# Performance work log

Measured on AMD Instinct MI355X. Metric: run time of the kernel, lower is better.

## Reference

```python
import jax, jax.numpy as jnp
import numpy as np

B, S, V, E, H, L = 2, 2048, 32000, 512, 8, 4
DH = E // H      # 64 head dim
M = 256          # FAVOR+ random features
CHUNK = 128      # causal prefix-sum chunk size


def setup_inputs() -> dict:
    key = jax.random.key(0)
    ks = jax.random.split(key, 12)
    init = lambda k, shape, s=0.02: (jax.random.normal(k, shape) * s).astype(jnp.float32)
    return {
        "src": jax.random.randint(ks[0], (B, S), 0, V),
        "tgt": jax.random.randint(ks[1], (B, S), 0, V),
        "emb": init(ks[2], (V, E), 1.0),
        "ln_emb_g": jnp.ones((E,), jnp.float32), "ln_emb_b": jnp.zeros((E,), jnp.float32),
        "Wq": init(ks[3], (L, E, E)), "Wk": init(ks[4], (L, E, E)),
        "Wv": init(ks[5], (L, E, E)), "Wo": init(ks[6], (L, E, E)),
        "ln1_g": jnp.ones((L, E), jnp.float32), "ln1_b": jnp.zeros((L, E), jnp.float32),
        "W1": init(ks[7], (L, E, 4 * E)), "b1": jnp.zeros((L, 4 * E), jnp.float32),
        "W2": init(ks[8], (L, 4 * E, E)), "b2": jnp.zeros((L, E), jnp.float32),
        "ln2_g": jnp.ones((L, E), jnp.float32), "ln2_b": jnp.zeros((L, E), jnp.float32),
        "proj": jax.random.normal(ks[9], (L, M, DH), dtype=jnp.float32),  # FAVOR+ projections (buffers)
        "fc_w": init(ks[10], (E, V)), "fc_b": jnp.zeros((V,), jnp.float32),
    }


def _ln(x, g, b, eps=1e-5):
    mu = jnp.mean(x, -1, keepdims=True)
    var = jnp.mean((x - mu) ** 2, -1, keepdims=True)
    return (x - mu) * jax.lax.rsqrt(var + eps) * g + b


def _posenc(s, e):
    pos = jnp.arange(s, dtype=jnp.float32)[:, None]
    div = jnp.exp(jnp.arange(0, e, 2, dtype=jnp.float32) * (-jnp.log(10000.0) / e))
    ang = pos * div                                   # [s, e/2]
    return jnp.stack([jnp.sin(ang), jnp.cos(ang)], -1).reshape(s, e)


def _features(x, proj, is_query):
    # FAVOR+ positive softmax-kernel random features. x: [b,h,s,d], proj: [m,d]
    dn = x.shape[-1] ** -0.25
    ratio = proj.shape[0] ** -0.5
    xd = jnp.einsum('bhsd,md->bhsm', x, proj) * dn
    diag = 0.5 * jnp.sum((x * dn) ** 2, -1)[..., None]
    mx = jnp.max(xd, -1, keepdims=True) if is_query else jnp.max(xd)
    return ratio * (jnp.exp(xd - diag - mx) + 1e-4)


def _causal_linear_attn(q, k, v):
    # q,k: [b,h,s,m] positive features; v: [b,h,s,d]. Chunked prefix-sum recurrence.
    b, h, s, m = q.shape
    d = v.shape[-1]
    nc = s // CHUNK
    rs = lambda t: t.reshape(b, h, nc, CHUNK, t.shape[-1]).transpose(2, 0, 1, 3, 4)

    def step(carry, inp):
        Ssum, zsum = carry                             # [b,h,m,d], [b,h,m]
        qc, kc, vc = inp                               # [b,h,c,m/ d]
        kv = jnp.einsum('bhcm,bhcd->bhcmd', kc, vc)
        Sc = Ssum[:, :, None] + jnp.cumsum(kv, axis=2)
        zc = zsum[:, :, None] + jnp.cumsum(kc, axis=2)
        num = jnp.einsum('bhcm,bhcmd->bhcd', qc, Sc)
        den = jnp.einsum('bhcm,bhcm->bhc', qc, zc)
        return (Sc[:, :, -1], zc[:, :, -1]), num / (den[..., None] + 1e-6)

    init = (jnp.zeros((b, h, m, d), q.dtype), jnp.zeros((b, h, m), q.dtype))
    _, outs = jax.lax.scan(step, init, (rs(q), rs(k), rs(v)))
    return outs.transpose(1, 2, 0, 3, 4).reshape(b, h, s, d)


def _forward(src, tgt, emb, ln_emb_g, ln_emb_b, Wq, Wk, Wv, Wo, ln1_g, ln1_b,
             W1, b1, W2, b2, ln2_g, ln2_b, proj, fc_w, fc_b):
    s = src.shape[1]
    pe = _posenc(s, E)
    x = emb[src] + pe                                 # [B,S,E]
    # tgt is embedded+normed in the original wrapper but the encoder-style Performer
    # only consumes its first (src) argument; masks default to None.
    _ = _ln(emb[tgt] + pe[: tgt.shape[1]], ln_emb_g, ln_emb_b)
    x = _ln(x, ln_emb_g, ln_emb_b)

    def layer(x, p):
        wq, wk, wv, wo, g1, bb1, w1, c1, w2, c2, g2, bb2, P = p
        h = _ln(x, g1, bb1)
        bsz, sl = h.shape[0], h.shape[1]
        split = lambda t: t.reshape(bsz, sl, H, DH).transpose(0, 2, 1, 3)  # [b,h,s,dh]
        q, k, v = split(h @ wq), split(h @ wk), split(h @ wv)
        qf = _features(q, P, True)
        kf = _features(k, P, False)
        o = _causal_linear_attn(qf, kf, v)
        o = o.transpose(0, 2, 1, 3).reshape(bsz, sl, E)
        x = x + o @ wo
        h2 = _ln(x, g2, bb2)
        x = x + jax.nn.gelu(h2 @ w1 + c1, approximate=False) @ w2 + c2
        return x, None

    x, _ = jax.lax.scan(layer, x, (Wq, Wk, Wv, Wo, ln1_g, ln1_b, W1, b1, W2, b2, ln2_g, ln2_b, proj))
    return x @ fc_w + fc_b                             # [B,S,V]


def reference(src, tgt, emb, ln_emb_g, ln_emb_b, Wq, Wk, Wv, Wo, ln1_g, ln1_b,
              W1, b1, W2, b2, ln2_g, ln2_b, proj, fc_w, fc_b):
    return _forward(src, tgt, emb, ln_emb_g, ln_emb_b, Wq, Wk, Wv, Wo, ln1_g, ln1_b,
                    W1, b1, W2, b2, ln2_g, ln2_b, proj, fc_w, fc_b)
```

## Files before the change

kernel.cpp:

```cpp
#include <hip/hip_runtime.h>
#include <math.h>

typedef unsigned short u16;
typedef unsigned int u32;
typedef __attribute__((ext_vector_type(8))) short bf16x8;
typedef __attribute__((ext_vector_type(4))) float f32x4;

constexpr int B_  = 2;
constexpr int S_  = 2048;
constexpr int V_  = 32000;
constexpr int E_  = 512;
constexpr int H_  = 8;
constexpr int L_  = 4;
constexpr int DH_ = 64;
constexpr int M_  = 256;
constexpr int CH_ = 128;
constexpr int NC_ = 16;
constexpr int NTOK_ = B_ * S_;
constexpr int KE_ = 3 * E_;
constexpr int KF_ = 3 * 4 * E_;

__device__ __forceinline__ float warp_sum64(float x) {
#pragma unroll
  for (int off = 32; off; off >>= 1) x += __shfl_xor(x, off);
  return x;
}
__device__ __forceinline__ float warp_max64(float x) {
#pragma unroll
  for (int off = 32; off; off >>= 1) x = fmaxf(x, __shfl_xor(x, off));
  return x;
}
__device__ __forceinline__ u16 bf16_rne(float x) {
  u32 u = __builtin_bit_cast(u32, x);
  u += 0x7fffu + ((u >> 16) & 1u);
  return (u16)(u >> 16);
}
__device__ __forceinline__ float bf16_f(u16 h) {
  u32 u = ((u32)h) << 16;
  return __builtin_bit_cast(float, u);
}
__device__ __forceinline__ void gload_lds16(const u16* g, u16* l) {
  __builtin_amdgcn_global_load_lds(
      (const __attribute__((address_space(1))) void*)g,
      (__attribute__((address_space(3))) void*)l, 16, 0, 0);
}
__device__ __forceinline__ void ext_write(u16* ro, int col, int seg, float v) {
  const u16 hi = bf16_rne(v);
  const u16 lo = bf16_rne(v - bf16_f(hi));
  ro[col] = hi; ro[seg + col] = hi; ro[2 * seg + col] = lo;
}

__global__ __launch_bounds__(256) void embed_ln_k(
    const int* __restrict__ src, const float* __restrict__ emb,
    const float* __restrict__ g, const float* __restrict__ bta,
    float* __restrict__ X) {
  __shared__ float red[4];
  const int row = blockIdx.x;
  const int s   = row & (S_ - 1);
  const int tid = threadIdx.x;
  const int tok = src[row];
  float v[2];
#pragma unroll
  for (int i = 0; i < 2; i++) {
    const int e = tid + i * 256;
    const float j = (float)(e & ~1);
    const float div = expf(j * (-9.210340371976184f / (float)E_));
    const float ang = (float)s * div;
    const float pe = (e & 1) ? cosf(ang) : sinf(ang);
    v[i] = emb[(size_t)tok * E_ + e] + pe;
  }
  float sum = warp_sum64(v[0] + v[1]);
  if ((tid & 63) == 0) red[tid >> 6] = sum;
  __syncthreads();
  const float mu = (red[0] + red[1] + red[2] + red[3]) * (1.f / E_);
  __syncthreads();
  const float d0 = v[0] - mu, d1 = v[1] - mu;
  float s2 = warp_sum64(d0 * d0 + d1 * d1);
  if ((tid & 63) == 0) red[tid >> 6] = s2;
  __syncthreads();
  const float var = (red[0] + red[1] + red[2] + red[3]) * (1.f / E_);
  const float r = rsqrtf(var + 1e-5f);
  X[(size_t)row * E_ + tid]       = d0 * r * g[tid] + bta[tid];
  X[(size_t)row * E_ + tid + 256] = d1 * r * g[tid + 256] + bta[tid + 256];
}

__global__ __launch_bounds__(256) void ln_rows_ext_k(
    const float* __restrict__ Xin, const float* __restrict__ g,
    const float* __restrict__ bta, u16* __restrict__ Eo) {
  __shared__ float red[4];
  const int row = blockIdx.x, tid = threadIdx.x;
  const float* xr = Xin + (size_t)row * E_;
  const float v0 = xr[tid], v1 = xr[tid + 256];
  float sum = warp_sum64(v0 + v1);
  if ((tid & 63) == 0) red[tid >> 6] = sum;
  __syncthreads();
  const float mu = (red[0] + red[1] + red[2] + red[3]) * (1.f / E_);
  __syncthreads();
  const float d0 = v0 - mu, d1 = v1 - mu;
  float s2 = warp_sum64(d0 * d0 + d1 * d1);
  if ((tid & 63) == 0) red[tid >> 6] = s2;
  __syncthreads();
  const float var = (red[0] + red[1] + red[2] + red[3]) * (1.f / E_);
  const float r = rsqrtf(var + 1e-5f);
  u16* ro = Eo + (size_t)row * KE_;
  ext_write(ro, tid,       E_, d0 * r * g[tid] + bta[tid]);
  ext_write(ro, tid + 256, E_, d1 * r * g[tid + 256] + bta[tid + 256]);
}

__global__ __launch_bounds__(256) void xconv_k(
    const float* __restrict__ X, u16* __restrict__ Eo) {
  const int row = blockIdx.x, tid = threadIdx.x;
  u16* ro = Eo + (size_t)row * KE_;
#pragma unroll
  for (int i = 0; i < 2; i++) {
    const int e = tid + i * 256;
    ext_write(ro, e, E_, X[(size_t)row * E_ + e]);
  }
}

__global__ __launch_bounds__(256) void convw_k(
    const float* __restrict__ W, u16* __restrict__ D, int K, int ldsrc) {
  __shared__ float t[32][33];
  const int tid = threadIdx.x;
  const int n0 = blockIdx.x * 32, k0 = blockIdx.y * 32;
  const int r = tid >> 5, c = tid & 31;
#pragma unroll
  for (int i = 0; i < 4; i++)
    t[r + i * 8][c] = W[(size_t)(k0 + r + i * 8) * ldsrc + n0 + c];
  __syncthreads();
#pragma unroll
  for (int i = 0; i < 4; i++) {
    const int nn = r + i * 8;
    const float v = t[c][nn];
    const u16 hi = bf16_rne(v);
    const u16 lo = bf16_rne(v - bf16_f(hi));
    u16* ro = D + (size_t)(n0 + nn) * (3 * K) + k0 + c;
    ro[0] = hi; ro[K] = lo; ro[2 * K] = hi;
  }
}

__global__ __launch_bounds__(256) void convw4_k(
    const float* __restrict__ p0, const float* __restrict__ p1,
    const float* __restrict__ p2, const float* __restrict__ p3,
    u16* __restrict__ D) {
  __shared__ float t[32][33];
  const int tid = threadIdx.x, z = blockIdx.z;
  const float* ps[4] = {p0, p1, p2, p3};
  const float* W = ps[z];
  u16* Dz = D + (size_t)z * E_ * KE_;
  const int n0 = blockIdx.x * 32, k0 = blockIdx.y * 32;
  const int r = tid >> 5, c = tid & 31;
#pragma unroll
  for (int i = 0; i < 4; i++)
    t[r + i * 8][c] = W[(size_t)(k0 + r + i * 8) * E_ + n0 + c];
  __syncthreads();
#pragma unroll
  for (int i = 0; i < 4; i++) {
    const int nn = r + i * 8;
    const float v = t[c][nn];
    const u16 hi = bf16_rne(v);
    const u16 lo = bf16_rne(v - bf16_f(hi));
    u16* ro = Dz + (size_t)(n0 + nn) * KE_ + k0 + c;
    ro[0] = hi; ro[E_] = lo; ro[2 * E_] = hi;
  }
}

template <int BM, bool BIAS, bool ACC, bool GEXT>
__global__ __launch_bounds__(256) void gemm_bf3(
    const u16* __restrict__ A, const u16* __restrict__ Bt,
    const float* __restrict__ bias, float* __restrict__ C,
    u16* __restrict__ Eo, int Kp, int ldC, int NE) {
  constexpr int BN = 128, BK = 64;
  constexpr int WROWS = BM / 64;
  constexpr int WCOLS = 4 / WROWS;
  constexpr int CW = BN / WCOLS;
  constexpr int MR = 4;
  constexpr int NR = CW / 16;
  __shared__ u16 Al[BM * BK];
  __shared__ u16 Bl[BN * BK];
  const int tid = threadIdx.x;
  const int wid = tid >> 6, lane = tid & 63;
  const int wr = wid / WCOLS, wc = wid % WCOLS;
  const int l15 = lane & 15, l4 = lane >> 4;
  const int bm = blockIdx.y * BM, bn = blockIdx.x * BN;
  f32x4 acc[MR][NR];
#pragma unroll
  for (int i = 0; i < MR; i++)
#pragma unroll
    for (int j = 0; j < NR; j++) acc[i][j] = (f32x4)(0.f);
  const int srow = tid >> 3;
  const int scol = (tid & 7) * 8;
  const u16* Abase = A + (size_t)(bm + srow) * Kp + scol;
  const u16* Bbase = Bt + (size_t)(bn + srow) * Kp + scol;
  for (int k0 = 0; k0 < Kp; k0 += BK) {
#pragma unroll
    for (int i = 0; i < BM / 32; i++)
      gload_lds16(Abase + (size_t)(i * 32) * Kp + k0, Al + i * 2048 + tid * 8);
#pragma unroll
    for (int i = 0; i < 4; i++)
      gload_lds16(Bbase + (size_t)(i * 32) * Kp + k0, Bl + i * 2048 + tid * 8);
    __syncthreads();
#pragma unroll
    for (int kk = 0; kk < BK; kk += 32) {
      bf16x8 af[MR], bfr[NR];
#pragma unroll
      for (int i = 0; i < MR; i++)
        af[i] = *reinterpret_cast<const bf16x8*>(
            &Al[(wr * 64 + i * 16 + l15) * BK + kk + l4 * 8]);
#pragma unroll
      for (int j = 0; j < NR; j++)
        bfr[j] = *reinterpret_cast<const bf16x8*>(
            &Bl[(wc * CW + j * 16 + l15) * BK + kk + l4 * 8]);
#pragma unroll
      for (int i = 0; i < MR; i++)
#pragma unroll
        for (int j = 0; j < NR; j++)
          acc[i][j] = __builtin_amdgcn_mfma_f32_16x16x32_bf16(
              af[i], bfr[j], acc[i][j], 0, 0, 0);
    }
    __syncthreads();
  }
#pragma unroll
  for (int i = 0; i < MR; i++) {
#pragma unroll
    for (int j = 0; j < NR; j++) {
#pragma unroll
      for (int r = 0; r < 4; r++) {
        const int row = bm + wr * 64 + i * 16 + l4 * 4 + r;
        const int col = bn + wc * CW + j * 16 + l15;
        float v = acc[i][j][r];
        if constexpr (BIAS) v += bias[col];
        if constexpr (GEXT) {
          v = 0.5f * v * (1.f + erff(v * 0.7071067811865475f));
          ext_write(Eo + (size_t)row * (3 * NE), col, NE, v);
        } else {
          const size_t ci = (size_t)row * ldC + col;
          if constexpr (ACC) C[ci] += v; else C[ci] = v;
        }
      }
    }
  }
}

__global__ __launch_bounds__(256) void feat_q_k(
    const float* __restrict__ Q, const float* __restrict__ P,
    float* __restrict__ QF) {
  __shared__ alignas(16) float qrow[64];
  __shared__ float red[4];
  const int tid = threadIdx.x, bx = blockIdx.x;
  const int st = bx & 255, h = (bx >> 8) & 7, b = bx >> 11;
  float4 preg[16];
#pragma unroll
  for (int i = 0; i < 16; i++)
    preg[i] = *reinterpret_cast<const float4*>(&P[(size_t)tid * DH_ + i * 4]);
  const float dn = 0.35355339059327373f;
  for (int ss = 0; ss < 8; ss++) {
    const int s = st * 8 + ss;
    if (tid < 64) qrow[tid] = Q[((size_t)(b * S_ + s)) * E_ + h * DH_ + tid];
    __syncthreads();
    float xd = 0.f, q2 = 0.f;
#pragma unroll
    for (int i = 0; i < 16; i++) {
      const float4 q4 = *reinterpret_cast<const float4*>(&qrow[i * 4]);
      xd += preg[i].x * q4.x + preg[i].y * q4.y + preg[i].z * q4.z + preg[i].w * q4.w;
      q2 += q4.x * q4.x + q4.y * q4.y + q4.z * q4.z + q4.w * q4.w;
    }
    xd *= dn;
    const float dg = 0.5f * dn * dn * q2;
    float mx = warp_max64(xd);
    if ((tid & 63) == 0) red[tid >> 6] = mx;
    __syncthreads();
    mx = fmaxf(fmaxf(red[0], red[1]), fmaxf(red[2], red[3]));
    QF[(((size_t)(b * H_ + h)) * S_ + s) * M_ + tid] =
        0.0625f * (expf(xd - dg - mx) + 1e-4f);
    __syncthreads();
  }
}

__global__ __launch_bounds__(256) void feat_k1_k(
    const float* __restrict__ K, const float* __restrict__ P,
    float* __restrict__ KF, float* __restrict__ DIAGK, float* __restrict__ PMAX) {
  __shared__ alignas(16) float krow[64];
  __shared__ float red[4];
  const int tid = threadIdx.x, bx = blockIdx.x;
  const int st = bx & 255, h = (bx >> 8) & 7, b = bx >> 11;
  float4 preg[16];
#pragma unroll
  for (int i = 0; i < 16; i++)
    preg[i] = *reinterpret_cast<const float4*>(&P[(size_t)tid * DH_ + i * 4]);
  const float dn = 0.35355339059327373f;
  float bmax = -3.0e38f;
  for (int ss = 0; ss < 8; ss++) {
    const int s = st * 8 + ss;
    if (tid < 64) krow[tid] = K[((size_t)(b * S_ + s)) * E_ + h * DH_ + tid];
    __syncthreads();
    float xd = 0.f, q2 = 0.f;
#pragma unroll
    for (int i = 0; i < 16; i++) {
      const float4 q4 = *reinterpret_cast<const float4*>(&krow[i * 4]);
      xd += preg[i].x * q4.x + preg[i].y * q4.y + preg[i].z * q4.z + preg[i].w * q4.w;
      q2 += q4.x * q4.x + q4.y * q4.y + q4.z * q4.z + q4.w * q4.w;
    }
    xd *= dn;
    const float dg = 0.5f * dn * dn * q2;
    const size_t ridx = ((size_t)(b * H_ + h)) * S_ + s;
    KF[ridx * M_ + tid] = xd;
    if (tid == 0) DIAGK[ridx] = dg;
    bmax = fmaxf(bmax, xd);
    __syncthreads();
  }
  bmax = warp_max64(bmax);
  if ((tid & 63) == 0) red[tid >> 6] = bmax;
  __syncthreads();
  if (tid == 0) PMAX[bx] = fmaxf(fmaxf(red[0], red[1]), fmaxf(red[2], red[3]));
}

__global__ __launch_bounds__(256) void maxred_k(
    const float* __restrict__ PM, int n, float* __restrict__ G) {
  __shared__ float w[4];
  const int tid = threadIdx.x;
  float v = -3.0e38f;
  for (int i = tid; i < n; i += 256) v = fmaxf(v, PM[i]);
  v = warp_max64(v);
  if ((tid & 63) == 0) w[tid >> 6] = v;
  __syncthreads();
  if (tid == 0) G[0] = fmaxf(fmaxf(w[0], w[1]), fmaxf(w[2], w[3]));
}

__global__ __launch_bounds__(256) void feat_k2_k(
    float* __restrict__ KF, const float* __restrict__ DIAG,
    const float* __restrict__ G) {
  const float gm = G[0];
  const size_t n = (size_t)B_ * H_ * S_ * M_;
  for (size_t i = (size_t)blockIdx.x * 256 + threadIdx.x; i < n;
       i += (size_t)gridDim.x * 256) {
    const float xd = KF[i];
    const float dg = DIAG[i >> 8];
    KF[i] = 0.0625f * (expf(xd - dg - gm) + 1e-4f);
  }
}

__global__ __launch_bounds__(256) void chunk_sums_k(
    const float* __restrict__ KF, const float* __restrict__ V,
    float* __restrict__ CSKV, float* __restrict__ CSZ) {
  __shared__ alignas(16) float vl[CH_ * DH_];
  const int tid = threadIdx.x, blk = blockIdx.x;
  const int c = blk & 15, h = (blk >> 4) & 7, b = blk >> 7;
  const int bh = b * H_ + h;
#pragma unroll
  for (int i = 0; i < 32; i++) {
    const int e = i * 256 + tid;
    vl[e] = V[((size_t)(b * S_ + c * CH_ + (e >> 6))) * E_ + h * DH_ + (e & 63)];
  }
  __syncthreads();
  float4 acc[16];
#pragma unroll
  for (int i = 0; i < 16; i++) acc[i] = make_float4(0.f, 0.f, 0.f, 0.f);
  float z = 0.f;
  const size_t kfbase = ((size_t)bh * S_ + c * CH_) * M_ + tid;
  for (int t = 0; t < CH_; t++) {
    const float kf = KF[kfbase + (size_t)t * M_];
    z += kf;
#pragma unroll
    for (int i = 0; i < 16; i++) {
      const float4 vv = *reinterpret_cast<const float4*>(&vl[t * DH_ + i * 4]);
      acc[i].x += kf * vv.x; acc[i].y += kf * vv.y;
      acc[i].z += kf * vv.z; acc[i].w += kf * vv.w;
    }
  }
  const size_t base = ((size_t)bh * NC_ + c) * (M_ * DH_) + (size_t)tid * DH_;
#pragma unroll
  for (int i = 0; i < 16; i++)
    *reinterpret_cast<float4*>(&CSKV[base + i * 4]) = acc[i];
  CSZ[((size_t)bh * NC_ + c) * M_ + tid] = z;
}

__global__ __launch_bounds__(256) void chunk_prefix_k(
    float* __restrict__ CSKV, float* __restrict__ CSZ) {
  const int tid = threadIdx.x, bx = blockIdx.x;
  const int ds = bx & 15, bh = bx >> 4;
  float run[4] = {0.f, 0.f, 0.f, 0.f};
  for (int c = 0; c < NC_; c++) {
    const size_t base = ((size_t)bh * NC_ + c) * (M_ * DH_) + ds * 1024;
#pragma unroll
    for (int i = 0; i < 4; i++) {
      const size_t idx = base + i * 256 + tid;
      const float t = CSKV[idx];
      CSKV[idx] = run[i];
      run[i] += t;
    }
  }
  if (ds == 0) {
    float zr = 0.f;
    for (int c = 0; c < NC_; c++) {
      const size_t idx = ((size_t)bh * NC_ + c) * M_ + tid;
      const float t = CSZ[idx];
      CSZ[idx] = zr;
      zr += t;
    }
  }
}

__global__ __launch_bounds__(256) void attn_out_k(
    const float* __restrict__ QF, const float* __restrict__ KF,
    const float* __restrict__ V, const float* __restrict__ CSKV,
    const float* __restrict__ CSZ, u16* __restrict__ Oe) {
  constexpr int DSP = 32;
  __shared__ alignas(16) float Sl[M_ * 36];
  __shared__ alignas(16) float qrow[M_];
  __shared__ alignas(16) float vrow[DSP];
  __shared__ float np[256];
  __shared__ float denp[4];
  const int tid = threadIdx.x, blk = blockIdx.x;
  const int dh = blk & 1, c = (blk >> 1) & 15, h = (blk >> 5) & 7, b = blk >> 8;
  const int bh = b * H_ + h;
  const size_t sbase = ((size_t)bh * NC_ + c) * (M_ * DH_) + dh * DSP;
#pragma unroll
  for (int i = 0; i < 32; i++) {
    const int e = i * 256 + tid;
    Sl[(e >> 5) * 36 + (e & 31)] = CSKV[sbase + (size_t)(e >> 5) * DH_ + (e & 31)];
  }
  float zreg = CSZ[((size_t)bh * NC_ + c) * M_ + tid];
  const int wid = tid >> 6, lane = tid & 63;
  __syncthreads();
  const size_t qkbase = ((size_t)bh * S_ + c * CH_) * M_;
  for (int t = 0; t < CH_; t++) {
    const int sg = c * CH_ + t;
    if (tid < DSP) vrow[tid] = V[((size_t)(b * S_ + sg)) * E_ + h * DH_ + dh * DSP + tid];
    qrow[tid] = QF[qkbase + (size_t)t * M_ + tid];
    const float kft = KF[qkbase + (size_t)t * M_ + tid];
    __syncthreads();
    zreg += kft;
    float* srow = &Sl[tid * 36];
#pragma unroll
    for (int i = 0; i < 8; i++) {
      float4 sv = *reinterpret_cast<float4*>(&srow[i * 4]);
      const float4 vv = *reinterpret_cast<const float4*>(&vrow[i * 4]);
      sv.x += kft * vv.x; sv.y += kft * vv.y;
      sv.z += kft * vv.z; sv.w += kft * vv.w;
      *reinterpret_cast<float4*>(&srow[i * 4]) = sv;
    }
    const float dp = warp_sum64(qrow[tid] * zreg);
    if (lane == 0) denp[wid] = dp;
    __syncthreads();
    {
      const int g = tid >> 5, d = tid & 31;
      float p = 0.f;
#pragma unroll
      for (int mm = 0; mm < 32; mm++)
        p += qrow[g * 32 + mm] * Sl[(g * 32 + mm) * 36 + d];
      np[g * 32 + d] = p;
    }
    __syncthreads();
    if (tid < DSP) {
      float num = 0.f;
#pragma unroll
      for (int g = 0; g < 8; g++) num += np[g * 32 + tid];
      const float den = denp[0] + denp[1] + denp[2] + denp[3];
      const float ov = num / (den + 1e-6f);
      const int cb = h * DH_ + dh * DSP + tid;
      ext_write(Oe + (size_t)(b * S_ + sg) * KE_, cb, E_, ov);
    }
  }
}

extern "C" void kernel_launch(void* const* d_in, const int* in_sizes, int n_in,
                              void* d_out, int out_size, void* d_ws, size_t ws_size,
                              hipStream_t stream) {
  const int*   src      = (const int*)d_in[0];
  const float* emb      = (const float*)d_in[2];
  const float* ln_emb_g = (const float*)d_in[3];
  const float* ln_emb_b = (const float*)d_in[4];
  const float* Wq       = (const float*)d_in[5];
  const float* Wk       = (const float*)d_in[6];
  const float* Wv       = (const float*)d_in[7];
  const float* Wo       = (const float*)d_in[8];
  const float* ln1_g    = (const float*)d_in[9];
  const float* ln1_b    = (const float*)d_in[10];
  const float* W1       = (const float*)d_in[11];
  const float* b1       = (const float*)d_in[12];
  const float* W2       = (const float*)d_in[13];
  const float* b2       = (const float*)d_in[14];
  const float* ln2_g    = (const float*)d_in[15];
  const float* ln2_b    = (const float*)d_in[16];
  const float* proj     = (const float*)d_in[17];
  const float* fc_w     = (const float*)d_in[18];
  const float* fc_b     = (const float*)d_in[19];
  float* out = (float*)d_out;
  float* ws  = (float*)d_ws;

  size_t off = 0;
  auto alloc = [&](size_t n) {
    float* p = ws + off;
    off += (n + 63) & ~(size_t)63;
    return p;
  };
  float* X    = alloc((size_t)NTOK_ * E_);
  float* Qb   = alloc((size_t)NTOK_ * E_);
  float* Kb   = alloc((size_t)NTOK_ * E_);
  float* Vb   = alloc((size_t)NTOK_ * E_);
  float* QF   = alloc((size_t)B_ * H_ * S_ * M_);
  float* KF   = alloc((size_t)B_ * H_ * S_ * M_);
  float* CSKV = alloc((size_t)B_ * H_ * NC_ * M_ * DH_);
  float* CSZ  = alloc((size_t)B_ * H_ * NC_ * M_);
  float* DIAGK= alloc((size_t)B_ * H_ * S_);
  float* PMAX = alloc(4096);
  float* GMAX = alloc(64);
  u16* Hext  = (u16*)alloc((size_t)NTOK_ * KE_ / 2);
  u16* Oext  = (u16*)alloc((size_t)NTOK_ * KE_ / 2);
  u16* Gext  = (u16*)alloc((size_t)NTOK_ * KF_ / 2);
  u16* WqkvoE= (u16*)alloc((size_t)4 * E_ * KE_ / 2);
  u16* W1E   = (u16*)alloc((size_t)(4 * E_) * KE_ / 2);
  u16* W2E   = (u16*)alloc((size_t)E_ * KF_ / 2);

  const dim3 blk256(256);
  const dim3 gQKV(E_ / 128, NTOK_ / 64);
  const dim3 gFFN1(4 * E_ / 128, NTOK_ / 128);

  embed_ln_k<<<NTOK_, blk256, 0, stream>>>(src, emb, ln_emb_g, ln_emb_b, X);

  for (int l = 0; l < L_; l++) {
    const float* Pl = proj + (size_t)l * M_ * DH_;
    convw4_k<<<dim3(E_ / 32, E_ / 32, 4), blk256, 0, stream>>>(
        Wq + (size_t)l * E_ * E_, Wk + (size_t)l * E_ * E_,
        Wv + (size_t)l * E_ * E_, Wo + (size_t)l * E_ * E_, WqkvoE);
    ln_rows_ext_k<<<NTOK_, blk256, 0, stream>>>(X, ln1_g + l * E_, ln1_b + l * E_, Hext);
    gemm_bf3<64, false, false, false><<<gQKV, blk256, 0, stream>>>(
        Hext, WqkvoE + (size_t)0 * E_ * KE_, nullptr, Qb, nullptr, KE_, E_, 0);
    gemm_bf3<64, false, false, false><<<gQKV, blk256, 0, stream>>>(
        Hext, WqkvoE + (size_t)1 * E_ * KE_, nullptr, Kb, nullptr, KE_, E_, 0);
    gemm_bf3<64, false, false, false><<<gQKV, blk256, 0, stream>>>(
        Hext, WqkvoE + (size_t)2 * E_ * KE_, nullptr, Vb, nullptr, KE_, E_, 0);
    feat_q_k<<<B_ * H_ * (S_ / 8), blk256, 0, stream>>>(Qb, Pl, QF);
    feat_k1_k<<<B_ * H_ * (S_ / 8), blk256, 0, stream>>>(Kb, Pl, KF, DIAGK, PMAX);
    maxred_k<<<1, blk256, 0, stream>>>(PMAX, B_ * H_ * (S_ / 8), GMAX);
    feat_k2_k<<<4096, blk256, 0, stream>>>(KF, DIAGK, GMAX);
    chunk_sums_k<<<B_ * H_ * NC_, blk256, 0, stream>>>(KF, Vb, CSKV, CSZ);
    chunk_prefix_k<<<B_ * H_ * 16, blk256, 0, stream>>>(CSKV, CSZ);
    attn_out_k<<<B_ * H_ * NC_ * 2, blk256, 0, stream>>>(QF, KF, Vb, CSKV, CSZ, Oext);
    gemm_bf3<64, false, true, false><<<gQKV, blk256, 0, stream>>>(
        Oext, WqkvoE + (size_t)3 * E_ * KE_, nullptr, X, nullptr, KE_, E_, 0);
    ln_rows_ext_k<<<NTOK_, blk256, 0, stream>>>(X, ln2_g + l * E_, ln2_b + l * E_, Hext);
    convw_k<<<dim3(4 * E_ / 32, E_ / 32), blk256, 0, stream>>>(
        W1 + (size_t)l * E_ * 4 * E_, W1E, E_, 4 * E_);
    gemm_bf3<128, true, false, true><<<gFFN1, blk256, 0, stream>>>(
        Hext, W1E, b1 + (size_t)l * 4 * E_, nullptr, Gext, KE_, 0, 4 * E_);
    convw_k<<<dim3(E_ / 32, 4 * E_ / 32), blk256, 0, stream>>>(
        W2 + (size_t)l * 4 * E_ * E_, W2E, 4 * E_, E_);
    gemm_bf3<64, true, true, false><<<gQKV, blk256, 0, stream>>>(
        Gext, W2E, b2 + (size_t)l * E_, X, nullptr, KF_, E_, 0);
  }
  xconv_k<<<NTOK_, blk256, 0, stream>>>(X, Hext);
  for (int sl = 0; sl < 2; sl++) {
    const int n0 = sl * 16000;
    convw_k<<<dim3(16000 / 32, E_ / 32), blk256, 0, stream>>>(
        fc_w + n0, Gext, E_, V_);
    gemm_bf3<128, true, false, false><<<dim3(16000 / 128, NTOK_ / 128), blk256, 0, stream>>>(
        Hext, Gext, fc_b + n0, out + n0, nullptr, KE_, V_, 0);
  }
}
```

Before: 4.125 ms.

## Rewrite causal attention output as chunked matmuls and swizzle GEMM block order

Replaces the per-timestep sequential attention-output kernel with a chunk-parallel formulation. It computes a masked intra-chunk Q·K^T score matrix, multiplies that by V, and adds Q times the prefix state, all as register-tiled shared-memory matmuls. This removes 128 serial steps, each with several barriers, per block, in exchange for more FLOPs and fewer blocks (256 instead of 512). It also adds an optional grouped block-index swizzle to the GEMM, enabled for FFN1 and the vocab projection, to improve L2 reuse of the B tiles.

```diff
diff --git a/kernel.cpp b/kernel.cpp
--- a/kernel.cpp
+++ b/kernel.cpp
@@ -165,7 +165,7 @@
   }
 }
 
-template <int BM, bool BIAS, bool ACC, bool GEXT>
+template <int BM, bool BIAS, bool ACC, bool GEXT, bool SWZ>
 __global__ __launch_bounds__(256) void gemm_bf3(
     const u16* __restrict__ A, const u16* __restrict__ Bt,
     const float* __restrict__ bias, float* __restrict__ C,
@@ -182,7 +182,26 @@
   const int wid = tid >> 6, lane = tid & 63;
   const int wr = wid / WCOLS, wc = wid % WCOLS;
   const int l15 = lane & 15, l4 = lane >> 4;
-  const int bm = blockIdx.y * BM, bn = blockIdx.x * BN;
+  int bxi = blockIdx.x, byi = blockIdx.y;
+  if constexpr (SWZ) {
+    const int nbx = gridDim.x, nby = gridDim.y;
+    const int lid = byi * nbx + bxi;
+    const int nfull = nbx >> 3;
+    const int pw = nby << 3;
+    const int fullb = nfull * pw;
+    if (lid < fullb) {
+      const int pg = lid / pw;
+      const int wi = lid - pg * pw;
+      byi = wi >> 3;
+      bxi = (pg << 3) + (wi & 7);
+    } else {
+      const int rem = lid - fullb;
+      const int tcw = nbx - (nfull << 3);
+      byi = rem / tcw;
+      bxi = (nfull << 3) + rem - byi * tcw;
+    }
+  }
+  const int bm = byi * BM, bn = bxi * BN;
   f32x4 acc[MR][NR];
 #pragma unroll
   for (int i = 0; i < MR; i++)
@@ -401,65 +420,160 @@
   }
 }
 
-__global__ __launch_bounds__(256) void attn_out_k(
+__global__ __launch_bounds__(256) void attn_mm_k(
     const float* __restrict__ QF, const float* __restrict__ KF,
     const float* __restrict__ V, const float* __restrict__ CSKV,
     const float* __restrict__ CSZ, u16* __restrict__ Oe) {
-  constexpr int DSP = 32;
-  __shared__ alignas(16) float Sl[M_ * 36];
-  __shared__ alignas(16) float qrow[M_];
-  __shared__ alignas(16) float vrow[DSP];
-  __shared__ float np[256];
-  __shared__ float denp[4];
+  constexpr int LDA = CH_ + 4;
+  constexpr int KOFF = 64 * LDA;
+  constexpr int SSOFF = 64 * LDA;
+  __shared__ alignas(16) float As[CH_ * LDA];
+  __shared__ alignas(16) float QK[2 * 64 * LDA];
+  __shared__ float zl[M_];
+  __shared__ float den[CH_];
+  __shared__ float denA[CH_ * 17];
   const int tid = threadIdx.x, blk = blockIdx.x;
-  const int dh = blk & 1, c = (blk >> 1) & 15, h = (blk >> 5) & 7, b = blk >> 8;
+  const int c = blk & 15, h = (blk >> 4) & 7, b = blk >> 7;
   const int bh = b * H_ + h;
-  const size_t sbase = ((size_t)bh * NC_ + c) * (M_ * DH_) + dh * DSP;
-#pragma unroll
-  for (int i = 0; i < 32; i++) {
-    const int e = i * 256 + tid;
-    Sl[(e >> 5) * 36 + (e & 31)] = CSKV[sbase + (size_t)(e >> 5) * DH_ + (e & 31)];
-  }
-  float zreg = CSZ[((size_t)bh * NC_ + c) * M_ + tid];
-  const int wid = tid >> 6, lane = tid & 63;
-  __syncthreads();
-  const size_t qkbase = ((size_t)bh * S_ + c * CH_) * M_;
-  for (int t = 0; t < CH_; t++) {
-    const int sg = c * CH_ + t;
-    if (tid < DSP) vrow[tid] = V[((size_t)(b * S_ + sg)) * E_ + h * DH_ + dh * DSP + tid];
-    qrow[tid] = QF[qkbase + (size_t)t * M_ + tid];
-    const float kft = KF[qkbase + (size_t)t * M_ + tid];
-    __syncthreads();
-    zreg += kft;
-    float* srow = &Sl[tid * 36];
-#pragma unroll
-    for (int i = 0; i < 8; i++) {
-      float4 sv = *reinterpret_cast<float4*>(&srow[i * 4]);
-      const float4 vv = *reinterpret_cast<const float4*>(&vrow[i * 4]);
-      sv.x += kft * vv.x; sv.y += kft * vv.y;
-      sv.z += kft * vv.z; sv.w += kft * vv.w;
-      *reinterpret_cast<float4*>(&srow[i * 4]) = sv;
-    }
-    const float dp = warp_sum64(qrow[tid] * zreg);
-    if (lane == 0) denp[wid] = dp;
-    __syncthreads();
+  const int row0 = c * CH_;
+  const size_t qkbase = ((size_t)bh * S_ + row0) * M_;
+  const int tr = tid >> 4, tc = tid & 15;
+  const int lr = tid >> 1, lq4 = (tid & 1) * 32;
+  zl[tid] = CSZ[((size_t)bh * NC_ + c) * M_ + tid];
+  float acc[8][8];
+#pragma unroll
+  for (int i = 0; i < 8; i++)
+#pragma unroll
+    for (int j = 0; j < 8; j++) acc[i][j] = 0.f;
+  float denq[8] = {0.f, 0.f, 0.f, 0.f, 0.f, 0.f, 0.f, 0.f};
+  for (int mt = 0; mt < 4; mt++) {
+    const float* qsrc = QF + qkbase + (size_t)lr * M_ + mt * 64 + lq4;
+    const float* ksrc = KF + qkbase + (size_t)lr * M_ + mt * 64 + lq4;
+#pragma unroll
+    for (int u = 0; u < 8; u++) {
+      const float4 q4 = *reinterpret_cast<const float4*>(qsrc + u * 4);
+      const float4 k4 = *reinterpret_cast<const float4*>(ksrc + u * 4);
+      const int m0 = lq4 + u * 4;
+      QK[(m0 + 0) * LDA + lr] = q4.x; QK[(m0 + 1) * LDA + lr] = q4.y;
+      QK[(m0 + 2) * LDA + lr] = q4.z; QK[(m0 + 3) * LDA + lr] = q4.w;
+      QK[KOFF + (m0 + 0) * LDA + lr] = k4.x; QK[KOFF + (m0 + 1) * LDA + lr] = k4.y;
+      QK[KOFF + (m0 + 2) * LDA + lr] = k4.z; QK[KOFF + (m0 + 3) * LDA + lr] = k4.w;
+    }
+    __syncthreads();
+#pragma unroll
+    for (int mm = 0; mm < 4; mm++) {
+      const int m = tc * 4 + mm;
+      const float zv = zl[mt * 64 + m];
+      float a[8];
+      *reinterpret_cast<float4*>(&a[0]) = *reinterpret_cast<const float4*>(&QK[m * LDA + tr * 8]);
+      *reinterpret_cast<float4*>(&a[4]) = *reinterpret_cast<const float4*>(&QK[m * LDA + tr * 8 + 4]);
+#pragma unroll
+      for (int r = 0; r < 8; r++) denq[r] += a[r] * zv;
+    }
+#pragma unroll 8
+    for (int mm = 0; mm < 64; mm++) {
+      float a[8], bb[8];
+      *reinterpret_cast<float4*>(&a[0]) = *reinterpret_cast<const float4*>(&QK[mm * LDA + tr * 8]);
+      *reinterpret_cast<float4*>(&a[4]) = *reinterpret_cast<const float4*>(&QK[mm * LDA + tr * 8 + 4]);
+      *reinterpret_cast<float4*>(&bb[0]) = *reinterpret_cast<const float4*>(&QK[KOFF + mm * LDA + tc * 8]);
+      *reinterpret_cast<float4*>(&bb[4]) = *reinterpret_cast<const float4*>(&QK[KOFF + mm * LDA + tc * 8 + 4]);
+#pragma unroll
+      for (int i = 0; i < 8; i++)
+#pragma unroll
+        for (int j = 0; j < 8; j++) acc[i][j] += a[i] * bb[j];
+    }
+    __syncthreads();
+  }
+#pragma unroll
+  for (int r = 0; r < 8; r++) {
+    const int i = tr * 8 + r;
+    float rs = denq[r];
+#pragma unroll
+    for (int jj = 0; jj < 8; jj++) {
+      const int j = tc * 8 + jj;
+      const float v = (j <= i) ? acc[r][jj] : 0.f;
+      As[j * LDA + i] = v;
+      rs += v;
+    }
+    denA[i * 17 + tc] = rs;
+  }
+  __syncthreads();
+  if (tid < CH_) {
+    float s = 0.f;
+#pragma unroll
+    for (int t = 0; t < 16; t++) s += denA[tid * 17 + t];
+    den[tid] = s + 1e-6f;
+  }
+  {
+    const float* vsrc = V + ((size_t)(b * S_ + row0 + lr)) * E_ + h * DH_ + lq4;
+#pragma unroll
+    for (int u = 0; u < 8; u++) {
+      const float4 v4 = *reinterpret_cast<const float4*>(vsrc + u * 4);
+      *reinterpret_cast<float4*>(&QK[lr * 68 + lq4 + u * 4]) = v4;
+    }
+  }
+  __syncthreads();
+  float num[8][4];
+#pragma unroll
+  for (int r = 0; r < 8; r++)
+#pragma unroll
+    for (int d = 0; d < 4; d++) num[r][d] = 0.f;
+#pragma unroll 8
+  for (int j = 0; j < CH_; j++) {
+    float a[8];
+    *reinterpret_cast<float4*>(&a[0]) = *reinterpret_cast<const float4*>(&As[j * LDA + tr * 8]);
+    *reinterpret_cast<float4*>(&a[4]) = *reinterpret_cast<const float4*>(&As[j * LDA + tr * 8 + 4]);
+    const float4 bv = *reinterpret_cast<const float4*>(&QK[j * 68 + tc * 4]);
+#pragma unroll
+    for (int r = 0; r < 8; r++) {
+      num[r][0] += a[r] * bv.x; num[r][1] += a[r] * bv.y;
+      num[r][2] += a[r] * bv.z; num[r][3] += a[r] * bv.w;
+    }
+  }
+  __syncthreads();
+  const size_t sbase = ((size_t)bh * NC_ + c) * (M_ * DH_);
+  for (int mt = 0; mt < 4; mt++) {
+    const float* qsrc = QF + qkbase + (size_t)lr * M_ + mt * 64 + lq4;
+#pragma unroll
+    for (int u = 0; u < 8; u++) {
+      const float4 q4 = *reinterpret_cast<const float4*>(qsrc + u * 4);
+      const int m0 = lq4 + u * 4;
+      QK[(m0 + 0) * LDA + lr] = q4.x; QK[(m0 + 1) * LDA + lr] = q4.y;
+      QK[(m0 + 2) * LDA + lr] = q4.z; QK[(m0 + 3) * LDA + lr] = q4.w;
+    }
     {
-      const int g = tid >> 5, d = tid & 31;
-      float p = 0.f;
-#pragma unroll
-      for (int mm = 0; mm < 32; mm++)
-        p += qrow[g * 32 + mm] * Sl[(g * 32 + mm) * 36 + d];
-      np[g * 32 + d] = p;
-    }
-    __syncthreads();
-    if (tid < DSP) {
-      float num = 0.f;
-#pragma unroll
-      for (int g = 0; g < 8; g++) num += np[g * 32 + tid];
-      const float den = denp[0] + denp[1] + denp[2] + denp[3];
-      const float ov = num / (den + 1e-6f);
-      const int cb = h * DH_ + dh * DSP + tid;
-      ext_write(Oe + (size_t)(b * S_ + sg) * KE_, cb, E_, ov);
+      const int lr2 = tid >> 2, lq2 = (tid & 3) * 16;
+      const float* ssrc = CSKV + sbase + (size_t)(mt * 64 + lr2) * DH_ + lq2;
+#pragma unroll
+      for (int u = 0; u < 4; u++) {
+        const float4 s4 = *reinterpret_cast<const float4*>(ssrc + u * 4);
+        *reinterpret_cast<float4*>(&QK[SSOFF + lr2 * 68 + lq2 + u * 4]) = s4;
+      }
+    }
+    __syncthreads();
+#pragma unroll 8
+    for (int mm = 0; mm < 64; mm++) {
+      float a[8];
+      *reinterpret_cast<float4*>(&a[0]) = *reinterpret_cast<const float4*>(&QK[mm * LDA + tr * 8]);
+      *reinterpret_cast<float4*>(&a[4]) = *reinterpret_cast<const float4*>(&QK[mm * LDA + tr * 8 + 4]);
+      const float4 sv = *reinterpret_cast<const float4*>(&QK[SSOFF + mm * 68 + tc * 4]);
+#pragma unroll
+      for (int r = 0; r < 8; r++) {
+        num[r][0] += a[r] * sv.x; num[r][1] += a[r] * sv.y;
+        num[r][2] += a[r] * sv.z; num[r][3] += a[r] * sv.w;
+      }
+    }
+    __syncthreads();
+  }
+#pragma unroll
+  for (int r = 0; r < 8; r++) {
+    const int i = tr * 8 + r;
+    const float dinv = 1.f / den[i];
+    u16* ro = Oe + (size_t)(b * S_ + row0 + i) * KE_;
+#pragma unroll
+    for (int dd = 0; dd < 4; dd++) {
+      const int d = tc * 4 + dd;
+      ext_write(ro, h * DH_ + d, E_, num[r][dd] * dinv);
     }
   }
 }
@@ -525,11 +639,11 @@
         Wq + (size_t)l * E_ * E_, Wk + (size_t)l * E_ * E_,
         Wv + (size_t)l * E_ * E_, Wo + (size_t)l * E_ * E_, WqkvoE);
     ln_rows_ext_k<<<NTOK_, blk256, 0, stream>>>(X, ln1_g + l * E_, ln1_b + l * E_, Hext);
-    gemm_bf3<64, false, false, false><<<gQKV, blk256, 0, stream>>>(
+    gemm_bf3<64, false, false, false, false><<<gQKV, blk256, 0, stream>>>(
         Hext, WqkvoE + (size_t)0 * E_ * KE_, nullptr, Qb, nullptr, KE_, E_, 0);
-    gemm_bf3<64, false, false, false><<<gQKV, blk256, 0, stream>>>(
+    gemm_bf3<64, false, false, false, false><<<gQKV, blk256, 0, stream>>>(
         Hext, WqkvoE + (size_t)1 * E_ * KE_, nullptr, Kb, nullptr, KE_, E_, 0);
-    gemm_bf3<64, false, false, false><<<gQKV, blk256, 0, stream>>>(
+    gemm_bf3<64, false, false, false, false><<<gQKV, blk256, 0, stream>>>(
         Hext, WqkvoE + (size_t)2 * E_ * KE_, nullptr, Vb, nullptr, KE_, E_, 0);
     feat_q_k<<<B_ * H_ * (S_ / 8), blk256, 0, stream>>>(Qb, Pl, QF);
     feat_k1_k<<<B_ * H_ * (S_ / 8), blk256, 0, stream>>>(Kb, Pl, KF, DIAGK, PMAX);
@@ -537,17 +651,17 @@
     feat_k2_k<<<4096, blk256, 0, stream>>>(KF, DIAGK, GMAX);
     chunk_sums_k<<<B_ * H_ * NC_, blk256, 0, stream>>>(KF, Vb, CSKV, CSZ);
     chunk_prefix_k<<<B_ * H_ * 16, blk256, 0, stream>>>(CSKV, CSZ);
-    attn_out_k<<<B_ * H_ * NC_ * 2, blk256, 0, stream>>>(QF, KF, Vb, CSKV, CSZ, Oext);
-    gemm_bf3<64, false, true, false><<<gQKV, blk256, 0, stream>>>(
+    attn_mm_k<<<B_ * H_ * NC_, blk256, 0, stream>>>(QF, KF, Vb, CSKV, CSZ, Oext);
+    gemm_bf3<64, false, true, false, false><<<gQKV, blk256, 0, stream>>>(
         Oext, WqkvoE + (size_t)3 * E_ * KE_, nullptr, X, nullptr, KE_, E_, 0);
     ln_rows_ext_k<<<NTOK_, blk256, 0, stream>>>(X, ln2_g + l * E_, ln2_b + l * E_, Hext);
     convw_k<<<dim3(4 * E_ / 32, E_ / 32), blk256, 0, stream>>>(
         W1 + (size_t)l * E_ * 4 * E_, W1E, E_, 4 * E_);
-    gemm_bf3<128, true, false, true><<<gFFN1, blk256, 0, stream>>>(
+    gemm_bf3<128, true, false, true, true><<<gFFN1, blk256, 0, stream>>>(
         Hext, W1E, b1 + (size_t)l * 4 * E_, nullptr, Gext, KE_, 0, 4 * E_);
     convw_k<<<dim3(E_ / 32, 4 * E_ / 32), blk256, 0, stream>>>(
         W2 + (size_t)l * 4 * E_ * E_, W2E, 4 * E_, E_);
-    gemm_bf3<64, true, true, false><<<gQKV, blk256, 0, stream>>>(
+    gemm_bf3<64, true, true, false, false><<<gQKV, blk256, 0, stream>>>(
         Gext, W2E, b2 + (size_t)l * E_, X, nullptr, KF_, E_, 0);
   }
   xconv_k<<<NTOK_, blk256, 0, stream>>>(X, Hext);
@@ -555,7 +669,7 @@
     const int n0 = sl * 16000;
     convw_k<<<dim3(16000 / 32, E_ / 32), blk256, 0, stream>>>(
         fc_w + n0, Gext, E_, V_);
-    gemm_bf3<128, true, false, false><<<dim3(16000 / 128, NTOK_ / 128), blk256, 0, stream>>>(
+    gemm_bf3<128, true, false, false, true><<<dim3(16000 / 128, NTOK_ / 128), blk256, 0, stream>>>(
         Hext, Gext, fc_b + n0, out + n0, nullptr, KE_, V_, 0);
   }
 }
```

Result: faster. 3.666 ms (-11.1%).
